# Optimization experiments

Measured on AMD Instinct MI355X. Metric: run time of the kernel, lower is better.

Reference implementation:

```python
import jax, jax.numpy as jnp
import numpy as np
from jax import lax

TAU = 2.0      # tau_s
V_TH = 0.5     # spike threshold
ALPHA = 2.0    # ATan surrogate width

@jax.custom_vjp
def spike_fn(v):
    return (v >= V_TH).astype(v.dtype)

def _spike_fwd(v):
    return spike_fn(v), v

def _spike_bwd(v, g):
    sg = (ALPHA / 2.0) / (1.0 + (jnp.pi / 2.0 * ALPHA * (v - V_TH)) ** 2)
    return (g * sg,)

spike_fn.defvjp(_spike_fwd, _spike_bwd)

T, B, S = 4, 128, 64
D_STATE = D_TAU = D_EVENT = 3136
FUSION, HIDDEN, LAST = 512, 512, 18

def setup_inputs() -> dict:
    key = jax.random.key(0)
    ks = jax.random.split(key, 10)
    def w(k, i, o):
        return jax.random.normal(k, (i, o), jnp.float32) / np.sqrt(i)
    return {
        'state_embedding': jax.random.normal(ks[0], (T, B, D_STATE), jnp.float32),
        'tau_embedding': jax.random.normal(ks[1], (T, B * S, D_TAU), jnp.float32),
        'eventspikes_embedding': jax.random.normal(ks[2], (T, B, D_EVENT), jnp.float32),
        'W_prox': w(ks[3], D_STATE, FUSION),
        'W_dist': w(ks[4], D_TAU, FUSION),
        'W_trunk': w(ks[5], D_EVENT, FUSION),
        'W1': w(ks[6], FUSION, HIDDEN),
        'b1': jnp.zeros((HIDDEN,), jnp.float32),
        'W2': w(ks[7], HIDDEN, LAST),
        'b2': jnp.zeros((LAST,), jnp.float32),
    }

def reference(state_embedding, tau_embedding, eventspikes_embedding,
              W_prox, W_dist, W_trunk, W1, b1, W2, b2):
    t_win, bsz, _ = state_embedding.shape
    ssz = tau_embedding.shape[1] // bsz
    fsz = W_prox.shape[1]
    hsz = W1.shape[1]

    def step(carry, xs):
        p, d, t, soma, lif_mem = carry
        se, te, ee = xs
        prox = (se @ W_prox)[:, None, :]              # [B,1,F]
        dist = (te @ W_dist).reshape(bsz, ssz, fsz)   # [B,S,F]
        trunk = (ee @ W_trunk)[:, None, :]            # [B,1,F]
        # multi-compartment LIF integration
        p = p + (prox - p) / TAU
        d = d + (dist - d) / TAU
        t = t + (trunk - t) / TAU
        soma = soma + (p * d + t - soma) / TAU        # [B,S,F]
        s = spike_fn(soma)
        soma = soma * (1.0 - s)
        emb = s.reshape(bsz * ssz, fsz)
        # _last: Linear -> LIF -> Linear
        h = emb @ W1 + b1
        lif_mem = lif_mem + (h - lif_mem) / TAU
        hs = spike_fn(lif_mem)
        lif_mem = lif_mem * (1.0 - hs)
        out = hs @ W2 + b2                            # [B*S, LAST]
        return (p, d, t, soma, lif_mem), out

    z = jnp.zeros
    init = (z((bsz, 1, fsz)), z((bsz, ssz, fsz)), z((bsz, 1, fsz)),
            z((bsz, ssz, fsz)), z((bsz * ssz, hsz)))
    _, outs = lax.scan(step, init, (state_embedding, tau_embedding, eventspikes_embedding))
    q = outs.mean(0)                                  # average over time window
    return q.reshape(bsz, ssz, -1).transpose(0, 2, 1)  # [B, LAST, S]
```

## Files before the change

kernel.cpp:

```cpp
#include <hip/hip_runtime.h>
#include <stdint.h>

typedef __attribute__((ext_vector_type(4))) float f32x4;

#define T_WIN 4
#define BSZ   128
#define SSZ   64
#define DDIM  3136
#define FDIM  512
#define HDIM  512
#define LDIM  18
#define ROWS  8192
#define KB    16

struct GArgs { const void* A; const float* B; float* C; int M; };

__device__ __forceinline__ void kchunk3136(int z, int& ks, int& ke) {
  ks = (z <= 7) ? 384 * z : 2912;
  ke = (z <= 6) ? 384 * (z + 1) : ((z == 7) ? 2912 : 3136);
}

template<int AMODE, int SMALLS>
__global__ __launch_bounds__(128, 2) void gemm_chunks(GArgs g0, GArgs g1, GArgs g2,
                                                      int N, int K, int kcmode) {
  const int chunk = gridDim.x >> 3;
  const int orig  = blockIdx.x;
  const int lin   = (orig & 7) * chunk + (orig >> 3);

  GArgs g = g0;
  int xb, y;
  if (SMALLS && lin >= 1024) {
    const int sidx = lin - 1024;
    g  = (sidx >> 4) ? g2 : g1;
    xb = (sidx >> 2) & 3;
    y  = sidx & 3;
  } else {
    xb = lin >> 2;
    y  = lin & 3;
  }

  int ks, ke;
  if (kcmode == 0) kchunk3136(blockIdx.z, ks, ke);
  else { ks = blockIdx.z * 256; ke = ks + 256; }

  const int m0 = xb * 128;
  const int n0 = y * 128;
  float* C = g.C + (size_t)blockIdx.z * g.M * N;

  __shared__ float sA[KB][128];
  __shared__ float sB[KB][132];

  const int tid = threadIdx.x;
  const int tx = tid & 15;
  const int ty = tid >> 4;

  const int am = tid;
  const int br = tid >> 3;
  const int bc = (tid & 7) * 16;

  const float*   Af = (const float*)g.A;
  const uint8_t* A8 = (const uint8_t*)g.A;

  float acc[16][8];
#pragma unroll
  for (int i = 0; i < 16; i++)
#pragma unroll
    for (int j = 0; j < 8; j++) acc[i][j] = 0.f;

  f32x4 av[4], bv[4];
  auto load_step = [&](int k0) {
    if (AMODE == 0) {
      const float* ap = Af + (size_t)(m0 + am) * K + k0;
#pragma unroll
      for (int c = 0; c < 4; c++) av[c] = *(const f32x4*)(ap + 4 * c);
    } else {
      uint4 wrd = *(const uint4*)(A8 + (size_t)(m0 + am) * K + k0);
      uint32_t u[4] = {wrd.x, wrd.y, wrd.z, wrd.w};
#pragma unroll
      for (int c = 0; c < 4; c++) {
        av[c][0] = (float)(u[c] & 255u);
        av[c][1] = (float)((u[c] >> 8) & 255u);
        av[c][2] = (float)((u[c] >> 16) & 255u);
        av[c][3] = (float)((u[c] >> 24) & 255u);
      }
    }
    const float* bp = g.B + (size_t)(k0 + br) * N + n0 + bc;
#pragma unroll
    for (int c = 0; c < 4; c++) bv[c] = *(const f32x4*)(bp + 4 * c);
  };

  load_step(ks);
  for (int k0 = ks; k0 < ke; k0 += KB) {
    __syncthreads();
#pragma unroll
    for (int c = 0; c < 4; c++)
#pragma unroll
      for (int j = 0; j < 4; j++)
        sA[4 * c + j][am] = av[c][j];
#pragma unroll
    for (int c = 0; c < 4; c++)
      *(f32x4*)&sB[br][bc + 4 * c] = bv[c];
    __syncthreads();

    if (k0 + KB < ke) load_step(k0 + KB);

#pragma unroll 4
    for (int k = 0; k < KB; k++) {
      f32x4 a0 = *(const f32x4*)&sA[k][ty * 16];
      f32x4 a1 = *(const f32x4*)&sA[k][ty * 16 + 4];
      f32x4 a2 = *(const f32x4*)&sA[k][ty * 16 + 8];
      f32x4 a3 = *(const f32x4*)&sA[k][ty * 16 + 12];
      f32x4 b0 = *(const f32x4*)&sB[k][tx * 4];
      f32x4 b1 = *(const f32x4*)&sB[k][64 + tx * 4];
      float a[16] = {a0[0], a0[1], a0[2], a0[3], a1[0], a1[1], a1[2], a1[3],
                     a2[0], a2[1], a2[2], a2[3], a3[0], a3[1], a3[2], a3[3]};
      float b[8]  = {b0[0], b0[1], b0[2], b0[3], b1[0], b1[1], b1[2], b1[3]};
#pragma unroll
      for (int i = 0; i < 16; i++)
#pragma unroll
        for (int j = 0; j < 8; j++)
          acc[i][j] = __fmaf_rn(a[i], b[j], acc[i][j]);
    }
  }

#pragma unroll
  for (int i = 0; i < 16; i++) {
    float* cp = C + (size_t)(m0 + ty * 16 + i) * N + n0;
    f32x4 v0 = {acc[i][0], acc[i][1], acc[i][2], acc[i][3]};
    f32x4 v1 = {acc[i][4], acc[i][5], acc[i][6], acc[i][7]};
    *(f32x4*)(cp + tx * 4) = v0;
    *(f32x4*)(cp + 64 + tx * 4) = v1;
  }
}

__global__ __launch_bounds__(256) void filter_pt9(const float* __restrict__ Cp,
                                                  const float* __restrict__ Ct,
                                                  float* __restrict__ P,
                                                  float* __restrict__ Tf) {
  const size_t CH = (size_t)T_WIN * BSZ * FDIM;
  int idx = blockIdx.x * 256 + threadIdx.x;
  int b = idx >> 7;
  int fc = (idx & 127) << 2;
  f32x4 p = {0.f, 0.f, 0.f, 0.f}, t = {0.f, 0.f, 0.f, 0.f};
  for (int tt = 0; tt < T_WIN; tt++) {
    size_t o = (size_t)(tt * BSZ + b) * FDIM + fc;
    f32x4 x = *(const f32x4*)&Cp[o];
    f32x4 y = *(const f32x4*)&Ct[o];
    for (int q = 1; q < 9; q++) {
      f32x4 xq = *(const f32x4*)&Cp[o + q * CH];
      f32x4 yq = *(const f32x4*)&Ct[o + q * CH];
#pragma unroll
      for (int c = 0; c < 4; c++) { x[c] = __fadd_rn(x[c], xq[c]); y[c] = __fadd_rn(y[c], yq[c]); }
    }
#pragma unroll
    for (int c = 0; c < 4; c++) {
      p[c] = __fadd_rn(p[c], __fmul_rn(__fsub_rn(x[c], p[c]), 0.5f));
      t[c] = __fadd_rn(t[c], __fmul_rn(__fsub_rn(y[c], t[c]), 0.5f));
    }
    *(f32x4*)&P[o] = p;
    *(f32x4*)&Tf[o] = t;
  }
}

__global__ __launch_bounds__(256) void lif_soma9(const float* __restrict__ Cd,
                                                 const float* __restrict__ P,
                                                 const float* __restrict__ Tf,
                                                 uint8_t* __restrict__ emb) {
  const size_t CH = (size_t)T_WIN * ROWS * FDIM;
  int idx = blockIdx.x * 256 + threadIdx.x;
  int r = idx >> 7;
  int fc = (idx & 127) << 2;
  int b = r >> 6;
  f32x4 d = {0.f, 0.f, 0.f, 0.f}, soma = {0.f, 0.f, 0.f, 0.f};
#pragma unroll
  for (int t = 0; t < T_WIN; t++) {
    size_t o = (size_t)(t * ROWS + r) * FDIM + fc;
    f32x4 x = *(const f32x4*)&Cd[o];
#pragma unroll
    for (int q = 1; q < 9; q++) {
      f32x4 xq = *(const f32x4*)&Cd[o + q * CH];
#pragma unroll
      for (int c = 0; c < 4; c++) x[c] = __fadd_rn(x[c], xq[c]);
    }
    f32x4 pv = *(const f32x4*)&P[(size_t)(t * BSZ + b) * FDIM + fc];
    f32x4 tv = *(const f32x4*)&Tf[(size_t)(t * BSZ + b) * FDIM + fc];
    uint32_t bits = 0;
#pragma unroll
    for (int c = 0; c < 4; c++) {
      d[c] = __fadd_rn(d[c], __fmul_rn(__fsub_rn(x[c], d[c]), 0.5f));
      float pd = __fmul_rn(pv[c], d[c]);
      float u  = __fadd_rn(pd, tv[c]);
      float w  = __fsub_rn(u, soma[c]);
      soma[c] = __fadd_rn(soma[c], __fmul_rn(w, 0.5f));
      if (soma[c] >= 0.5f) { bits |= (1u << (8 * c)); soma[c] = 0.f; }
    }
    *(uint32_t*)&emb[o] = bits;
  }
}

__global__ __launch_bounds__(256) void lif_hidden2(const float* __restrict__ Hc,
                                                   const float* __restrict__ b1,
                                                   uint8_t* __restrict__ cnt) {
  const size_t CH = (size_t)T_WIN * ROWS * FDIM;
  int idx = blockIdx.x * 256 + threadIdx.x;
  int r = idx >> 7;
  int fc = (idx & 127) << 2;
  f32x4 bb = *(const f32x4*)&b1[fc];
  f32x4 lif = {0.f, 0.f, 0.f, 0.f};
  uint32_t counts = 0;
#pragma unroll
  for (int t = 0; t < T_WIN; t++) {
    size_t o = (size_t)(t * ROWS + r) * FDIM + fc;
    f32x4 h0 = *(const f32x4*)&Hc[o];
    f32x4 h1 = *(const f32x4*)&Hc[o + CH];
#pragma unroll
    for (int c = 0; c < 4; c++) {
      float hv = __fadd_rn(__fadd_rn(h0[c], h1[c]), bb[c]);
      lif[c] = __fadd_rn(lif[c], __fmul_rn(__fsub_rn(hv, lif[c]), 0.5f));
      if (lif[c] >= 0.5f) { counts += (1u << (8 * c)); lif[c] = 0.f; }
    }
  }
  *(uint32_t*)&cnt[(size_t)r * FDIM + fc] = counts;
}

__global__ __launch_bounds__(256) void out_kernel(const uint8_t* __restrict__ cnt,
                                                  const float* __restrict__ W2,
                                                  const float* __restrict__ b2,
                                                  float* __restrict__ out) {
  int idx = blockIdx.x * 256 + threadIdx.x;
  int r = idx / LDIM;
  int j = idx - r * LDIM;
  const uint4* crow = (const uint4*)(cnt + (size_t)r * HDIM);
  float acc = 0.f;
  for (int q = 0; q < HDIM / 16; q++) {
    uint4 wrd = crow[q];
    uint32_t u[4] = {wrd.x, wrd.y, wrd.z, wrd.w};
#pragma unroll
    for (int wq = 0; wq < 4; wq++)
#pragma unroll
      for (int s = 0; s < 4; s++) {
        uint32_t c = (u[wq] >> (8 * s)) & 255u;
        if (c) acc = __fmaf_rn((float)c * 0.25f, W2[(16 * q + 4 * wq + s) * LDIM + j], acc);
      }
  }
  int b = r >> 6, s = r & 63;
  out[(size_t)b * (LDIM * SSZ) + j * SSZ + s] = __fadd_rn(acc, b2[j]);
}


extern "C" void kernel_launch(void* const* d_in, const int* in_sizes, int n_in,
                              void* d_out, int out_size, void* d_ws, size_t ws_size,
                              hipStream_t stream) {
  const float* se     = (const float*)d_in[0];
  const float* te     = (const float*)d_in[1];
  const float* ee     = (const float*)d_in[2];
  const float* Wprox  = (const float*)d_in[3];
  const float* Wdist  = (const float*)d_in[4];
  const float* Wtrunk = (const float*)d_in[5];
  const float* W1     = (const float*)d_in[6];
  const float* b1     = (const float*)d_in[7];
  const float* W2     = (const float*)d_in[8];
  const float* b2     = (const float*)d_in[9];

  char* ws = (char*)d_ws;
  float*   Cd   = (float*)(ws);
  float*   Hc   = (float*)(ws);
  float*   Cp   = (float*)(ws + 603979776);
  float*   Ct   = (float*)(ws + 613416960);
  float*   P    = (float*)(ws + 622854144);
  float*   Tf   = (float*)(ws + 623902720);
  uint8_t* emb8 = (uint8_t*)(ws + 624951296);
  uint8_t* cnt8 = (uint8_t*)(ws + 641728512);

  GArgs gd{te, Wdist, Cd, T_WIN * ROWS};
  GArgs gp{se, Wprox, Cp, T_WIN * BSZ};
  GArgs gt{ee, Wtrunk, Ct, T_WIN * BSZ};
  gemm_chunks<0, 1><<<dim3(1056, 1, 9), 128, 0, stream>>>(gd, gp, gt, FDIM, DDIM, 0);

  filter_pt9<<<64, 256, 0, stream>>>(Cp, Ct, P, Tf);

  lif_soma9<<<4096, 256, 0, stream>>>(Cd, P, Tf, emb8);

  GArgs gh{emb8, W1, Hc, T_WIN * ROWS};
  gemm_chunks<1, 0><<<dim3(1024, 1, 2), 128, 0, stream>>>(gh, gh, gh, HDIM, FDIM, 1);

  lif_hidden2<<<4096, 256, 0, stream>>>(Hc, b1, cnt8);

  out_kernel<<<576, 256, 0, stream>>>(cnt8, W2, b2, (float*)d_out);
}
```

Before: 2.029 ms.

## Double-buffer GEMM shared memory and load B tiles directly to LDS

Replaces the single-buffered sA/sB tiles with a double-buffered shared array. B is now staged into LDS with asynchronous global_load_lds_dwordx4, and A is prefetched two steps ahead. This removes one barrier per k-step and lets the next tile's loads overlap the FMA loop. In exchange it uses twice the LDS, relies on inline asm with m0 handling and vmcnt waits, and drops the padded B row, so bank conflicts may return.

```diff
diff --git a/kernel.cpp b/kernel.cpp
--- a/kernel.cpp
+++ b/kernel.cpp
@@ -42,21 +42,20 @@
   int ks, ke;
   if (kcmode == 0) kchunk3136(blockIdx.z, ks, ke);
   else { ks = blockIdx.z * 256; ke = ks + 256; }
+  const int NT = (ke - ks) / KB;
 
   const int m0 = xb * 128;
   const int n0 = y * 128;
   float* C = g.C + (size_t)blockIdx.z * g.M * N;
 
-  __shared__ float sA[KB][128];
-  __shared__ float sB[KB][132];
+  __shared__ float smem[8192];
 
   const int tid = threadIdx.x;
   const int tx = tid & 15;
   const int ty = tid >> 4;
-
   const int am = tid;
-  const int br = tid >> 3;
-  const int bc = (tid & 7) * 16;
+  const int lane = tid & 63;
+  const int wv   = tid >> 6;
 
   const float*   Af = (const float*)g.A;
   const uint8_t* A8 = (const uint8_t*)g.A;
@@ -67,8 +66,8 @@
 #pragma unroll
     for (int j = 0; j < 8; j++) acc[i][j] = 0.f;
 
-  f32x4 av[4], bv[4];
-  auto load_step = [&](int k0) {
+  f32x4 av[4];
+  auto load_A = [&](int k0) {
     if (AMODE == 0) {
       const float* ap = Af + (size_t)(m0 + am) * K + k0;
 #pragma unroll
@@ -84,34 +83,59 @@
         av[c][3] = (float)((u[c] >> 24) & 255u);
       }
     }
-    const float* bp = g.B + (size_t)(k0 + br) * N + n0 + bc;
-#pragma unroll
-    for (int c = 0; c < 4; c++) bv[c] = *(const f32x4*)(bp + 4 * c);
   };
 
-  load_step(ks);
-  for (int k0 = ks; k0 < ke; k0 += KB) {
-    __syncthreads();
+  const int bkk = lane >> 5;
+  const int bnn = (lane & 31) * 4;
+  auto stage_B = [&](int nb, int k0) {
+#pragma unroll
+    for (int r = 0; r < 4; r++) {
+      const int c = r * 2 + wv;
+      const float* gp = g.B + (size_t)(k0 + c * 2 + bkk) * N + n0 + bnn;
+      uint32_t m0v = (uint32_t)((4096 + nb * 2048 + c * 256) * 4);
+      m0v = __builtin_amdgcn_readfirstlane(m0v);
+      asm volatile("s_mov_b32 m0, %0\n\t"
+                   "global_load_lds_dwordx4 %1, off\n\t"
+                   :: "s"(m0v), "v"(gp) : "memory");
+    }
+  };
+
+  auto write_A = [&](int nb) {
+    const int abase = nb * 2048;
 #pragma unroll
     for (int c = 0; c < 4; c++)
 #pragma unroll
       for (int j = 0; j < 4; j++)
-        sA[4 * c + j][am] = av[c][j];
-#pragma unroll
-    for (int c = 0; c < 4; c++)
-      *(f32x4*)&sB[br][bc + 4 * c] = bv[c];
-    __syncthreads();
-
-    if (k0 + KB < ke) load_step(k0 + KB);
+        smem[abase + (4 * c + j) * 128 + am] = av[c][j];
+  };
+
+  load_A(ks);
+  stage_B(0, ks);
+  write_A(0);
+  load_A(ks + KB);
+  asm volatile("s_waitcnt vmcnt(0)" ::: "memory");
+  __syncthreads();
+
+  for (int it = 0; it < NT; ++it) {
+    const int k0 = ks + it * KB;
+    const int abase = (it & 1) * 2048;
+    const int bbase = 4096 + (it & 1) * 2048;
+
+    if (it + 1 < NT) {
+      const int nb = (it + 1) & 1;
+      stage_B(nb, k0 + KB);
+      write_A(nb);
+      if (it + 2 < NT) load_A(k0 + 2 * KB);
+    }
 
 #pragma unroll 4
     for (int k = 0; k < KB; k++) {
-      f32x4 a0 = *(const f32x4*)&sA[k][ty * 16];
-      f32x4 a1 = *(const f32x4*)&sA[k][ty * 16 + 4];
-      f32x4 a2 = *(const f32x4*)&sA[k][ty * 16 + 8];
-      f32x4 a3 = *(const f32x4*)&sA[k][ty * 16 + 12];
-      f32x4 b0 = *(const f32x4*)&sB[k][tx * 4];
-      f32x4 b1 = *(const f32x4*)&sB[k][64 + tx * 4];
+      f32x4 a0 = *(const f32x4*)&smem[abase + k * 128 + ty * 16];
+      f32x4 a1 = *(const f32x4*)&smem[abase + k * 128 + ty * 16 + 4];
+      f32x4 a2 = *(const f32x4*)&smem[abase + k * 128 + ty * 16 + 8];
+      f32x4 a3 = *(const f32x4*)&smem[abase + k * 128 + ty * 16 + 12];
+      f32x4 b0 = *(const f32x4*)&smem[bbase + k * 128 + tx * 4];
+      f32x4 b1 = *(const f32x4*)&smem[bbase + k * 128 + 64 + tx * 4];
       float a[16] = {a0[0], a0[1], a0[2], a0[3], a1[0], a1[1], a1[2], a1[3],
                      a2[0], a2[1], a2[2], a2[3], a3[0], a3[1], a3[2], a3[3]};
       float b[8]  = {b0[0], b0[1], b0[2], b0[3], b1[0], b1[1], b1[2], b1[3]};
@@ -121,6 +145,9 @@
         for (int j = 0; j < 8; j++)
           acc[i][j] = __fmaf_rn(a[i], b[j], acc[i][j]);
     }
+
+    asm volatile("s_waitcnt vmcnt(0)" ::: "memory");
+    __syncthreads();
   }
 
 #pragma unroll
```

New measurement: 2.068 ms. About the same (+1.9%).
